# Performance work log

Measured on AMD Instinct MI355X. Metric: run time of the kernel, lower is better.

The kernel has to match this reference:

```python
import jax, jax.numpy as jnp
import numpy as np

NEG_INF = -1000000000.0
B, N, D, H, L, DFF = 4, 1024, 512, 8, 6, 2048
DH = D // H
R2 = 10.0 ** 2  # locality_radius^2
EPS = 1e-5


def setup_inputs() -> dict:
    key = jax.random.key(0)
    ks = jax.random.split(key, 16)
    s = 0.02
    inp = {
        "tokens": jax.random.normal(ks[0], (B, N, D), jnp.float32),
        "xy": jax.random.uniform(ks[1], (B, N, 2), jnp.float32) * 100.0,
        "Wq": jax.random.normal(ks[2], (L, D, D), jnp.float32) * s,
        "Wk": jax.random.normal(ks[3], (L, D, D), jnp.float32) * s,
        "Wv": jax.random.normal(ks[4], (L, D, D), jnp.float32) * s,
        "Wo": jax.random.normal(ks[5], (L, D, D), jnp.float32) * s,
        "bo": jnp.zeros((L, D), jnp.float32),
        "W1": jax.random.normal(ks[6], (L, D, DFF), jnp.float32) * s,
        "b1": jnp.zeros((L, DFF), jnp.float32),
        "W2": jax.random.normal(ks[7], (L, DFF, D), jnp.float32) * s,
        "b2": jnp.zeros((L, D), jnp.float32),
        "g1": jnp.ones((L, D), jnp.float32),
        "be1": jnp.zeros((L, D), jnp.float32),
        "g2": jnp.ones((L, D), jnp.float32),
        "be2": jnp.zeros((L, D), jnp.float32),
        "gf": jnp.ones((D,), jnp.float32),
        "bf": jnp.zeros((D,), jnp.float32),
        "alive": jax.random.randint(ks[8], (B, N), 0, 2, dtype=jnp.int32),
        "species": jax.random.randint(ks[9], (B, N), 0, 3, dtype=jnp.int32),
        "n_agents": 512,
    }
    return inp


def _ln(x, g, b):
    m = jnp.mean(x, axis=-1, keepdims=True)
    v = jnp.mean((x - m) ** 2, axis=-1, keepdims=True)
    return (x - m) * jax.lax.rsqrt(v + EPS) * g + b


def _build_bias(alive, xy, species, dtype):
    # (B,1,N,N) additive bias, broadcast over heads (original repeats per head)
    af = alive.astype(dtype)
    bias = (1.0 - af)[:, None, None, :] * NEG_INF  # dead keys
    d2 = jnp.sum((xy[:, :, None, :] - xy[:, None, :, :]) ** 2, axis=-1)  # (B,N,N)
    bias = bias + jnp.where(d2 > R2, NEG_INF, 0.0)[:, None, :, :]
    ia = species < 2
    ip = species == 2
    ct = (ia[:, :, None] & ip[:, None, :]) | (ip[:, :, None] & ia[:, None, :])
    bias = bias + jnp.where(ct, NEG_INF, 0.0)[:, None, :, :]
    return bias


def reference(tokens, xy, Wq, Wk, Wv, Wo, bo, W1, b1, W2, b2,
              g1, be1, g2, be2, gf, bf, alive, species, n_agents):
    bias = _build_bias(alive, xy, species, tokens.dtype)
    scale = np.float32(np.sqrt(DH))
    x = tokens
    for l in range(L):
        h = _ln(x, g1[l], be1[l])
        q = (h @ Wq[l]).reshape(B, N, H, DH)
        k = (h @ Wk[l]).reshape(B, N, H, DH)
        v = (h @ Wv[l]).reshape(B, N, H, DH)
        scores = jnp.einsum('bihd,bjhd->bhij', q, k) / scale + bias
        w = jax.nn.softmax(scores, axis=-1)
        o = jnp.einsum('bhij,bjhd->bihd', w, v).reshape(B, N, D)
        x = x + (o @ Wo[l] + bo[l])
        h2 = _ln(x, g2[l], be2[l])
        ff = jax.nn.gelu(h2 @ W1[l] + b1[l], approximate=False) @ W2[l] + b2[l]
        x = x + ff
    return _ln(x, gf, bf)
```

## Files before the change

kernel.cpp:

```cpp
#include <hip/hip_runtime.h>
#include <math.h>

namespace {

constexpr int B = 4, N = 1024, D = 512, H = 8, DHd = 64, L = 6, DFFd = 2048;
constexpr int M = B * N;
constexpr int QKVS = 3 * D;
constexpr float NEG = -1000000000.0f;
constexpr float R2c = 100.0f;

typedef __attribute__((ext_vector_type(8))) short bf16x8;
typedef __attribute__((ext_vector_type(4))) float f32x4;
typedef __attribute__((ext_vector_type(16))) float f32x16;

__device__ __forceinline__ short f2bf(float f) {
  union { float f; unsigned u; } c; c.f = f;
  unsigned r = (c.u + 0x7fffu + ((c.u >> 16) & 1u)) >> 16;
  return (short)r;
}

__device__ __forceinline__ float gelu_f(float x) {
  return 0.5f * x * (1.0f + erff(x * 0.70710678118654752f));
}

__global__ __launch_bounds__(256) void bias_kernel(
    const float* __restrict__ xy, const int* __restrict__ alive,
    const int* __restrict__ species, float* __restrict__ bias)
{
  int j = blockIdx.x * 256 + threadIdx.x;
  int i = blockIdx.y;
  int b = blockIdx.z;
  float xi = xy[((size_t)b * N + i) * 2 + 0];
  float yi = xy[((size_t)b * N + i) * 2 + 1];
  float xj = xy[((size_t)b * N + j) * 2 + 0];
  float yj = xy[((size_t)b * N + j) * 2 + 1];
  float dx = xi - xj, dy = yi - yj;
  float d2 = dx * dx + dy * dy;
  float bv = 0.0f;
  if (alive[b * N + j] == 0) bv += NEG;
  if (d2 > R2c) bv += NEG;
  int si = species[b * N + i], sj = species[b * N + j];
  bool ia = si < 2, ip = si == 2, ja = sj < 2, jp = sj == 2;
  if ((ia && jp) || (ip && ja)) bv += NEG;
  bias[((size_t)b * N + i) * N + j] = bv;
}

__global__ __launch_bounds__(256) void wprep_kernel(
    const float* __restrict__ src, short* __restrict__ dst,
    int K, int Nc, size_t srcLS, size_t dstLS)
{
  __shared__ float t[32][33];
  int k0 = blockIdx.x * 32, n0 = blockIdx.y * 32;
  src += (size_t)blockIdx.z * srcLS;
  dst += (size_t)blockIdx.z * dstLS;
  int r = threadIdx.x >> 5, c = threadIdx.x & 31;
#pragma unroll
  for (int i = 0; i < 4; ++i)
    t[r + i * 8][c] = src[(size_t)(k0 + r + i * 8) * Nc + n0 + c];
  __syncthreads();
#pragma unroll
  for (int i = 0; i < 4; ++i)
    dst[(size_t)(n0 + r + i * 8) * K + k0 + c] = f2bf(t[c][r + i * 8]);
}

__global__ __launch_bounds__(64) void ln_kernel(
    const float* __restrict__ x, const float* __restrict__ g,
    const float* __restrict__ be, float* __restrict__ outf,
    short* __restrict__ outb)
{
  int row = blockIdx.x;
  int tid = threadIdx.x;
  const float* xr = x + (size_t)row * D;
  float v[8];
  float sum = 0.f;
#pragma unroll
  for (int i = 0; i < 8; ++i) { v[i] = xr[tid + i * 64]; sum += v[i]; }
#pragma unroll
  for (int off = 32; off > 0; off >>= 1) sum += __shfl_down(sum, off);
  sum = __shfl(sum, 0);
  float mean = sum * (1.0f / D);
  float vs = 0.f;
#pragma unroll
  for (int i = 0; i < 8; ++i) { float d = v[i] - mean; vs += d * d; }
#pragma unroll
  for (int off = 32; off > 0; off >>= 1) vs += __shfl_down(vs, off);
  vs = __shfl(vs, 0);
  float rstd = rsqrtf(vs * (1.0f / D) + 1e-5f);
#pragma unroll
  for (int i = 0; i < 8; ++i) {
    int c = tid + i * 64;
    float o = (v[i] - mean) * rstd * g[c] + be[c];
    if (outb) outb[(size_t)row * D + c] = f2bf(o);
    else      outf[(size_t)row * D + c] = o;
  }
}

__global__ __launch_bounds__(256, 2) void gemm_sk_kernel(
    const short* __restrict__ A, const short* __restrict__ Bt,
    const float* __restrict__ bvec, float* __restrict__ Cf,
    short* __restrict__ Cb, int K, int Nc, int mode)
{
  __shared__ __align__(16) char smem[4 * 17408];
  const int bm = blockIdx.y * 64, bn = blockIdx.x * 64;
  const int t = threadIdx.x, wave = t >> 6, lane = t & 63;
  const int half = lane >> 5;
  const int l32 = lane & 31;
  const int srow4 = lane >> 2, sseg4 = lane & 3;

  char* slot = smem + wave * 17408;
  const int kw0 = wave * (K >> 2);
  const int nch = K >> 7;

  const short* Ab = A + (size_t)(bm + srow4) * K + kw0 + sseg4 * 8;
  const short* Bb = Bt + (size_t)(bn + srow4) * K + kw0 + sseg4 * 8;

  auto issue = [&](int p, int kc) {
    char* ab = slot + p * 8192;
    char* bb = slot + p * 8192 + 4096;
#pragma unroll
    for (int i = 0; i < 4; ++i) {
      __builtin_amdgcn_global_load_lds(
          (const __attribute__((address_space(1))) void*)(Ab + (size_t)i * 16 * K + kc),
          (__attribute__((address_space(3))) void*)(ab + i * 1024), 16, 0, 0);
    }
#pragma unroll
    for (int i = 0; i < 4; ++i) {
      __builtin_amdgcn_global_load_lds(
          (const __attribute__((address_space(1))) void*)(Bb + (size_t)i * 16 * K + kc),
          (__attribute__((address_space(3))) void*)(bb + i * 1024), 16, 0, 0);
    }
  };

  f32x16 acc[2][2];
#pragma unroll
  for (int i = 0; i < 2; ++i)
#pragma unroll
    for (int j = 0; j < 2; ++j)
#pragma unroll
      for (int r = 0; r < 16; ++r) acc[i][j][r] = 0.f;

  issue(0, 0);
  for (int c = 0; c < nch; ++c) {
    const int p = c & 1;
    if (c + 1 < nch) {
      issue(p ^ 1, (c + 1) * 32);
      asm volatile("s_waitcnt vmcnt(%0)" :: "i"(8) : "memory");
    } else {
      asm volatile("s_waitcnt vmcnt(0)" ::: "memory");
    }
    const short* As = (const short*)(slot + p * 8192);
    const short* Bs = (const short*)(slot + p * 8192 + 4096);
#pragma unroll
    for (int ks = 0; ks < 2; ++ks) {
      bf16x8 a0 = *(const bf16x8*)&As[(l32) * 32 + ks * 16 + half * 8];
      bf16x8 a1 = *(const bf16x8*)&As[(32 + l32) * 32 + ks * 16 + half * 8];
      bf16x8 b0 = *(const bf16x8*)&Bs[(l32) * 32 + ks * 16 + half * 8];
      bf16x8 b1 = *(const bf16x8*)&Bs[(32 + l32) * 32 + ks * 16 + half * 8];
      acc[0][0] = __builtin_amdgcn_mfma_f32_32x32x16_bf16(a0, b0, acc[0][0], 0, 0, 0);
      acc[0][1] = __builtin_amdgcn_mfma_f32_32x32x16_bf16(a0, b1, acc[0][1], 0, 0, 0);
      acc[1][0] = __builtin_amdgcn_mfma_f32_32x32x16_bf16(a1, b0, acc[1][0], 0, 0, 0);
      acc[1][1] = __builtin_amdgcn_mfma_f32_32x32x16_bf16(a1, b1, acc[1][1], 0, 0, 0);
    }
  }

  float* red = (float*)slot;
#pragma unroll
  for (int ti = 0; ti < 2; ++ti)
#pragma unroll
    for (int tj = 0; tj < 2; ++tj)
#pragma unroll
      for (int r = 0; r < 16; ++r) {
        int row = ti * 32 + (r & 3) + 8 * (r >> 2) + 4 * half;
        red[row * 68 + tj * 32 + l32] = acc[ti][tj][r];
      }
  __syncthreads();

  const int row = t >> 2, cs = (t & 3) * 16;
  const size_t orow = (size_t)(bm + row) * Nc + bn + cs;
#pragma unroll
  for (int u = 0; u < 4; ++u) {
    float4 s0 = *(const float4*)((const float*)(smem + 0 * 17408) + row * 68 + cs + u * 4);
    float4 s1 = *(const float4*)((const float*)(smem + 1 * 17408) + row * 68 + cs + u * 4);
    float4 s2 = *(const float4*)((const float*)(smem + 2 * 17408) + row * 68 + cs + u * 4);
    float4 s3 = *(const float4*)((const float*)(smem + 3 * 17408) + row * 68 + cs + u * 4);
    float o0 = s0.x + s1.x + s2.x + s3.x;
    float o1 = s0.y + s1.y + s2.y + s3.y;
    float o2 = s0.z + s1.z + s2.z + s3.z;
    float o3 = s0.w + s1.w + s2.w + s3.w;
    const int col = bn + cs + u * 4;
    if (mode == 0) {
      short4 w = {f2bf(o0), f2bf(o1), f2bf(o2), f2bf(o3)};
      *(short4*)&Cb[orow + u * 4] = w;
    } else if (mode == 1) {
      float4 bv = *(const float4*)&bvec[col];
      float4 rv = *(const float4*)&Cf[orow + u * 4];
      float4 w = {o0 + bv.x + rv.x, o1 + bv.y + rv.y, o2 + bv.z + rv.z, o3 + bv.w + rv.w};
      *(float4*)&Cf[orow + u * 4] = w;
    } else {
      float4 bv = *(const float4*)&bvec[col];
      short4 w = {f2bf(gelu_f(o0 + bv.x)), f2bf(gelu_f(o1 + bv.y)),
                  f2bf(gelu_f(o2 + bv.z)), f2bf(gelu_f(o3 + bv.w))};
      *(short4*)&Cb[orow + u * 4] = w;
    }
  }
}

__global__ __launch_bounds__(256) void attn_mfma_kernel(
    const short* __restrict__ qkv, const float* __restrict__ bias,
    short* __restrict__ o)
{
  constexpr int LDR = 72;
  __shared__ __align__(16) short Qs[64 * LDR];
  __shared__ __align__(16) short Ks[2][64 * LDR];
  __shared__ __align__(16) short Vt[2][64 * LDR];
  __shared__ __align__(16) short Ps[4 * 16 * LDR];

  const int q0 = blockIdx.x * 64;
  const int hh = blockIdx.y;
  const int b  = blockIdx.z;
  const int t  = threadIdx.x;
  const int wave = t >> 6;
  const int lane = t & 63;
  const int quad = lane >> 4;
  const int ln16 = lane & 15;
  const int srow = t >> 2, sseg = t & 3;

  {
    const short* qb = qkv + (size_t)(b * N + q0 + srow) * QKVS + hh * 64 + sseg * 16;
    *(bf16x8*)&Qs[srow * LDR + sseg * 16] = *(const bf16x8*)qb;
    *(bf16x8*)&Qs[srow * LDR + sseg * 16 + 8] = *(const bf16x8*)(qb + 8);
  }
  __syncthreads();

  const int qrow = wave * 16 + ln16;
  const bf16x8 qf0 = *(const bf16x8*)&Qs[qrow * LDR + quad * 8];
  const bf16x8 qf1 = *(const bf16x8*)&Qs[qrow * LDR + 32 + quad * 8];

  float m_run = -1e30f, l_run = 0.f;
  f32x4 Oacc[4];
#pragma unroll
  for (int dt = 0; dt < 4; ++dt) Oacc[dt] = (f32x4){0.f, 0.f, 0.f, 0.f};

  short* Psw = Ps + wave * 16 * LDR;
  const float* brow = bias + (size_t)(b * N + q0 + wave * 16 + ln16) * N;
  const short* kb0 = qkv + (size_t)b * N * QKVS + 512 + hh * 64 + sseg * 16;
  const short* vb0 = qkv + (size_t)b * N * QKVS + 1024 + hh * 64 + sseg * 16;

  bf16x8 k0r = *(const bf16x8*)(kb0 + (size_t)srow * QKVS);
  bf16x8 k1r = *(const bf16x8*)(kb0 + (size_t)srow * QKVS + 8);
  bf16x8 v0r = *(const bf16x8*)(vb0 + (size_t)srow * QKVS);
  bf16x8 v1r = *(const bf16x8*)(vb0 + (size_t)srow * QKVS + 8);
  float4 b4[4];
#pragma unroll
  for (int ks = 0; ks < 4; ++ks)
    b4[ks] = *(const float4*)&brow[ks * 16 + quad * 4];

  for (int kt = 0; kt < 16; ++kt) {
    const int p = kt & 1;
    *(bf16x8*)&Ks[p][srow * LDR + sseg * 16] = k0r;
    *(bf16x8*)&Ks[p][srow * LDR + sseg * 16 + 8] = k1r;
#pragma unroll
    for (int e = 0; e < 8; ++e) {
      Vt[p][(sseg * 16 + e) * LDR + srow] = v0r[e];
      Vt[p][(sseg * 16 + 8 + e) * LDR + srow] = v1r[e];
    }
    const int k0n = (kt + 1 < 16) ? (kt + 1) * 64 : 0;
    bf16x8 nk0 = *(const bf16x8*)(kb0 + (size_t)(k0n + srow) * QKVS);
    bf16x8 nk1 = *(const bf16x8*)(kb0 + (size_t)(k0n + srow) * QKVS + 8);
    bf16x8 nv0 = *(const bf16x8*)(vb0 + (size_t)(k0n + srow) * QKVS);
    bf16x8 nv1 = *(const bf16x8*)(vb0 + (size_t)(k0n + srow) * QKVS + 8);
    float4 bcur[4] = {b4[0], b4[1], b4[2], b4[3]};
#pragma unroll
    for (int ks = 0; ks < 4; ++ks)
      b4[ks] = *(const float4*)&brow[k0n + ks * 16 + quad * 4];
    asm volatile("s_waitcnt lgkmcnt(0)\n\ts_barrier" ::: "memory");

    float sv[4][4];
#pragma unroll
    for (int ks = 0; ks < 4; ++ks) {
      bf16x8 a0 = *(const bf16x8*)&Ks[p][(ks * 16 + ln16) * LDR + quad * 8];
      bf16x8 a1 = *(const bf16x8*)&Ks[p][(ks * 16 + ln16) * LDR + 32 + quad * 8];
      f32x4 z = (f32x4){0.f, 0.f, 0.f, 0.f};
      z = __builtin_amdgcn_mfma_f32_16x16x32_bf16(a0, qf0, z, 0, 0, 0);
      z = __builtin_amdgcn_mfma_f32_16x16x32_bf16(a1, qf1, z, 0, 0, 0);
#pragma unroll
      for (int r = 0; r < 4; ++r)
        sv[ks][r] = z[r] * 0.125f + (&bcur[ks].x)[r];
    }

    float mt = sv[0][0];
#pragma unroll
    for (int ks = 0; ks < 4; ++ks)
#pragma unroll
      for (int r = 0; r < 4; ++r) mt = fmaxf(mt, sv[ks][r]);
    mt = fmaxf(mt, __shfl_xor(mt, 16));
    mt = fmaxf(mt, __shfl_xor(mt, 32));
    const float m_new = fmaxf(m_run, mt);
    const float alpha = __expf(m_run - m_new);
    m_run = m_new;
    float rs = 0.f;
    float pv[4][4];
#pragma unroll
    for (int ks = 0; ks < 4; ++ks)
#pragma unroll
      for (int r = 0; r < 4; ++r) {
        float e = __expf(sv[ks][r] - m_new);
        pv[ks][r] = e;
        rs += e;
      }
    rs += __shfl_xor(rs, 16);
    rs += __shfl_xor(rs, 32);
    l_run = l_run * alpha + rs;
    float af[4];
#pragma unroll
    for (int r = 0; r < 4; ++r) af[r] = __shfl(alpha, quad * 4 + r);
#pragma unroll
    for (int dt = 0; dt < 4; ++dt)
#pragma unroll
      for (int r = 0; r < 4; ++r) Oacc[dt][r] *= af[r];

#pragma unroll
    for (int ks = 0; ks < 4; ++ks) {
      short4 pk = {f2bf(pv[ks][0]), f2bf(pv[ks][1]), f2bf(pv[ks][2]), f2bf(pv[ks][3])};
      *(short4*)&Psw[ln16 * LDR + ks * 16 + quad * 4] = pk;
    }

    bf16x8 ap0 = *(const bf16x8*)&Psw[ln16 * LDR + quad * 8];
    bf16x8 ap1 = *(const bf16x8*)&Psw[ln16 * LDR + 32 + quad * 8];
#pragma unroll
    for (int dt = 0; dt < 4; ++dt) {
      bf16x8 bv0 = *(const bf16x8*)&Vt[p][(dt * 16 + ln16) * LDR + quad * 8];
      bf16x8 bv1 = *(const bf16x8*)&Vt[p][(dt * 16 + ln16) * LDR + 32 + quad * 8];
      Oacc[dt] = __builtin_amdgcn_mfma_f32_16x16x32_bf16(ap0, bv0, Oacc[dt], 0, 0, 0);
      Oacc[dt] = __builtin_amdgcn_mfma_f32_16x16x32_bf16(ap1, bv1, Oacc[dt], 0, 0, 0);
    }

    k0r = nk0; k1r = nk1; v0r = nv0; v1r = nv1;
  }

  const float linv = 1.0f / l_run;
  float iv[4];
#pragma unroll
  for (int r = 0; r < 4; ++r) iv[r] = __shfl(linv, quad * 4 + r);
#pragma unroll
  for (int dt = 0; dt < 4; ++dt) {
#pragma unroll
    for (int r = 0; r < 4; ++r) {
      int row = q0 + wave * 16 + quad * 4 + r;
      o[(size_t)(b * N + row) * D + hh * 64 + dt * 16 + ln16] =
          f2bf(Oacc[dt][r] * iv[r]);
    }
  }
}

}

extern "C" void kernel_launch(void* const* d_in, const int* in_sizes, int n_in,
                              void* d_out, int out_size, void* d_ws, size_t ws_size,
                              hipStream_t stream)
{
  const float* tokens  = (const float*)d_in[0];
  const float* xy      = (const float*)d_in[1];
  const float* Wq      = (const float*)d_in[2];
  const float* Wk      = (const float*)d_in[3];
  const float* Wv      = (const float*)d_in[4];
  const float* Wo      = (const float*)d_in[5];
  const float* bo      = (const float*)d_in[6];
  const float* W1      = (const float*)d_in[7];
  const float* b1      = (const float*)d_in[8];
  const float* W2      = (const float*)d_in[9];
  const float* b2      = (const float*)d_in[10];
  const float* g1      = (const float*)d_in[11];
  const float* be1     = (const float*)d_in[12];
  const float* g2      = (const float*)d_in[13];
  const float* be2     = (const float*)d_in[14];
  const float* gf      = (const float*)d_in[15];
  const float* bf      = (const float*)d_in[16];
  const int*   alive   = (const int*)d_in[17];
  const int*   species = (const int*)d_in[18];

  char* p = (char*)d_ws;
  float* bias = (float*)p; p += (size_t)B * N * N * 4;
  float* x    = (float*)p; p += (size_t)M * D * 4;
  short* h    = (short*)p; p += (size_t)M * D * 2;
  short* qkv  = (short*)p; p += (size_t)M * DFFd * 2;
  short* ff   = qkv;
  short* Wqkvt = (short*)p; p += (size_t)L * QKVS * D * 2;
  short* Wot   = (short*)p; p += (size_t)L * D * D * 2;
  short* W1t   = (short*)p; p += (size_t)L * DFFd * D * 2;
  short* W2t   = (short*)p; p += (size_t)L * D * DFFd * 2;

  hipMemcpyAsync(x, tokens, sizeof(float) * (size_t)M * D,
                 hipMemcpyDeviceToDevice, stream);
  bias_kernel<<<dim3(N / 256, N, B), 256, 0, stream>>>(xy, alive, species, bias);

  wprep_kernel<<<dim3(16, 16, L), 256, 0, stream>>>(
      Wq, Wqkvt + (size_t)0 * D * D, D, D, (size_t)D * D, (size_t)QKVS * D);
  wprep_kernel<<<dim3(16, 16, L), 256, 0, stream>>>(
      Wk, Wqkvt + (size_t)1 * D * D, D, D, (size_t)D * D, (size_t)QKVS * D);
  wprep_kernel<<<dim3(16, 16, L), 256, 0, stream>>>(
      Wv, Wqkvt + (size_t)2 * D * D, D, D, (size_t)D * D, (size_t)QKVS * D);
  wprep_kernel<<<dim3(16, 16, L), 256, 0, stream>>>(
      Wo, Wot, D, D, (size_t)D * D, (size_t)D * D);
  wprep_kernel<<<dim3(16, 64, L), 256, 0, stream>>>(
      W1, W1t, D, DFFd, (size_t)D * DFFd, (size_t)DFFd * D);
  wprep_kernel<<<dim3(64, 16, L), 256, 0, stream>>>(
      W2, W2t, DFFd, D, (size_t)DFFd * D, (size_t)D * DFFd);

  for (int l = 0; l < L; ++l) {
    ln_kernel<<<M, 64, 0, stream>>>(x, g1 + l * D, be1 + l * D, nullptr, h);
    gemm_sk_kernel<<<dim3(QKVS / 64, M / 64), 256, 0, stream>>>(
        h, Wqkvt + (size_t)l * QKVS * D, nullptr, nullptr, qkv, D, QKVS, 0);
    attn_mfma_kernel<<<dim3(N / 64, H, B), 256, 0, stream>>>(qkv, bias, h);
    gemm_sk_kernel<<<dim3(D / 64, M / 64), 256, 0, stream>>>(
        h, Wot + (size_t)l * D * D, bo + l * D, x, nullptr, D, D, 1);
    ln_kernel<<<M, 64, 0, stream>>>(x, g2 + l * D, be2 + l * D, nullptr, h);
    gemm_sk_kernel<<<dim3(DFFd / 64, M / 64), 256, 0, stream>>>(
        h, W1t + (size_t)l * DFFd * D, b1 + l * DFFd, nullptr, ff, D, DFFd, 2);
    gemm_sk_kernel<<<dim3(D / 64, M / 64), 256, 0, stream>>>(
        ff, W2t + (size_t)l * D * DFFd, b2 + l * D, x, nullptr, DFFd, D, 1);
  }
  ln_kernel<<<M, 64, 0, stream>>>(x, gf, bf, (float*)d_out, nullptr);
}
```

Baseline: 992.3 us.

## Fuse prep kernels, swizzle GEMM LDS, remap workgroups for XCD locality

Merges the weight transpose/convert kernels, the bias build and the token copy into one prep launch. Adds an XOR swizzle to the GEMM's LDS tile layout to cut bank conflicts on fragment reads. Remaps GEMM and attention workgroup indices so neighbouring tiles land on the same XCD for better L2 reuse. Packs four LayerNorm rows per 256-thread block. Costs are extra index arithmetic and a large branchy prep kernel.

```diff
diff --git a/kernel.cpp b/kernel.cpp
--- a/kernel.cpp
+++ b/kernel.cpp
@@ -3,7 +3,7 @@
 
 namespace {
 
-constexpr int B = 4, N = 1024, D = 512, H = 8, DHd = 64, L = 6, DFFd = 2048;
+constexpr int B = 4, N = 1024, D = 512, H = 8, L = 6, DFFd = 2048;
 constexpr int M = B * N;
 constexpr int QKVS = 3 * D;
 constexpr float NEG = -1000000000.0f;
@@ -23,53 +23,79 @@
   return 0.5f * x * (1.0f + erff(x * 0.70710678118654752f));
 }
 
-__global__ __launch_bounds__(256) void bias_kernel(
+__global__ __launch_bounds__(256) void prep_kernel(
+    const float* __restrict__ Wq, const float* __restrict__ Wk,
+    const float* __restrict__ Wv, const float* __restrict__ Wo,
+    const float* __restrict__ W1, const float* __restrict__ W2,
+    short* __restrict__ Wqkvt, short* __restrict__ Wot,
+    short* __restrict__ W1t, short* __restrict__ W2t,
     const float* __restrict__ xy, const int* __restrict__ alive,
-    const int* __restrict__ species, float* __restrict__ bias)
+    const int* __restrict__ species, float* __restrict__ bias,
+    const float* __restrict__ tokens, float* __restrict__ x)
 {
-  int j = blockIdx.x * 256 + threadIdx.x;
-  int i = blockIdx.y;
-  int b = blockIdx.z;
-  float xi = xy[((size_t)b * N + i) * 2 + 0];
-  float yi = xy[((size_t)b * N + i) * 2 + 1];
-  float xj = xy[((size_t)b * N + j) * 2 + 0];
-  float yj = xy[((size_t)b * N + j) * 2 + 1];
-  float dx = xi - xj, dy = yi - yj;
-  float d2 = dx * dx + dy * dy;
-  float bv = 0.0f;
-  if (alive[b * N + j] == 0) bv += NEG;
-  if (d2 > R2c) bv += NEG;
-  int si = species[b * N + i], sj = species[b * N + j];
-  bool ia = si < 2, ip = si == 2, ja = sj < 2, jp = sj == 2;
-  if ((ia && jp) || (ip && ja)) bv += NEG;
-  bias[((size_t)b * N + i) * N + j] = bv;
-}
-
-__global__ __launch_bounds__(256) void wprep_kernel(
-    const float* __restrict__ src, short* __restrict__ dst,
-    int K, int Nc, size_t srcLS, size_t dstLS)
-{
-  __shared__ float t[32][33];
-  int k0 = blockIdx.x * 32, n0 = blockIdx.y * 32;
-  src += (size_t)blockIdx.z * srcLS;
-  dst += (size_t)blockIdx.z * dstLS;
-  int r = threadIdx.x >> 5, c = threadIdx.x & 31;
-#pragma unroll
-  for (int i = 0; i < 4; ++i)
-    t[r + i * 8][c] = src[(size_t)(k0 + r + i * 8) * Nc + n0 + c];
-  __syncthreads();
-#pragma unroll
-  for (int i = 0; i < 4; ++i)
-    dst[(size_t)(n0 + r + i * 8) * K + k0 + c] = f2bf(t[c][r + i * 8]);
-}
-
-__global__ __launch_bounds__(64) void ln_kernel(
+  __shared__ float tt[32][33];
+  const int blk = blockIdx.x;
+  const int t = threadIdx.x;
+
+  if (blk < 18432) {
+    const float* src; short* dst; int K, Nc, tx; size_t srcLS, dstLS; int lb;
+    if (blk < 6144) {
+      const int w = blk / 1536; lb = blk % 1536; tx = 16; K = 512; Nc = 512;
+      srcLS = (size_t)D * D;
+      if (w == 0)      { src = Wq; dst = Wqkvt; dstLS = (size_t)QKVS * D; }
+      else if (w == 1) { src = Wk; dst = Wqkvt + (size_t)D * D; dstLS = (size_t)QKVS * D; }
+      else if (w == 2) { src = Wv; dst = Wqkvt + (size_t)2 * D * D; dstLS = (size_t)QKVS * D; }
+      else             { src = Wo; dst = Wot; dstLS = (size_t)D * D; }
+    } else if (blk < 12288) {
+      lb = blk - 6144; tx = 16; K = 512; Nc = DFFd;
+      src = W1; dst = W1t; srcLS = (size_t)D * DFFd; dstLS = (size_t)DFFd * D;
+    } else {
+      lb = blk - 12288; tx = 64; K = DFFd; Nc = 512;
+      src = W2; dst = W2t; srcLS = (size_t)DFFd * D; dstLS = (size_t)D * DFFd;
+    }
+    const int per = (K / 32) * (Nc / 32);
+    const int z = lb / per, rem = lb % per;
+    const int k0 = (rem % tx) * 32, n0 = (rem / tx) * 32;
+    src += (size_t)z * srcLS; dst += (size_t)z * dstLS;
+    const int r = t >> 5, c = t & 31;
+#pragma unroll
+    for (int i = 0; i < 4; ++i)
+      tt[r + i * 8][c] = src[(size_t)(k0 + r + i * 8) * Nc + n0 + c];
+    __syncthreads();
+#pragma unroll
+    for (int i = 0; i < 4; ++i)
+      dst[(size_t)(n0 + r + i * 8) * K + k0 + c] = f2bf(tt[c][r + i * 8]);
+  } else if (blk < 34816) {
+    const int e = blk - 18432;
+    const int j = (e & 3) * 256 + t;
+    const int i = (e >> 2) & 1023;
+    const int b = e >> 12;
+    float xi = xy[((size_t)b * N + i) * 2 + 0];
+    float yi = xy[((size_t)b * N + i) * 2 + 1];
+    float xj = xy[((size_t)b * N + j) * 2 + 0];
+    float yj = xy[((size_t)b * N + j) * 2 + 1];
+    float dx = xi - xj, dy = yi - yj;
+    float d2 = dx * dx + dy * dy;
+    float bv = 0.0f;
+    if (alive[b * N + j] == 0) bv += NEG;
+    if (d2 > R2c) bv += NEG;
+    int si = species[b * N + i], sj = species[b * N + j];
+    bool ia = si < 2, ip = si == 2, ja = sj < 2, jp = sj == 2;
+    if ((ia && jp) || (ip && ja)) bv += NEG;
+    bias[((size_t)b * N + i) * N + j] = bv;
+  } else {
+    const size_t e = (size_t)(blk - 34816) * 256 + t;
+    ((float4*)x)[e] = ((const float4*)tokens)[e];
+  }
+}
+
+__global__ __launch_bounds__(256) void ln_kernel(
     const float* __restrict__ x, const float* __restrict__ g,
     const float* __restrict__ be, float* __restrict__ outf,
     short* __restrict__ outb)
 {
-  int row = blockIdx.x;
-  int tid = threadIdx.x;
+  int row = blockIdx.x * 4 + (threadIdx.x >> 6);
+  int tid = threadIdx.x & 63;
   const float* xr = x + (size_t)row * D;
   float v[8];
   float sum = 0.f;
@@ -101,11 +127,16 @@
     short* __restrict__ Cb, int K, int Nc, int mode)
 {
   __shared__ __align__(16) char smem[4 * 17408];
-  const int bm = blockIdx.y * 64, bn = blockIdx.x * 64;
+  const int gx = gridDim.x;
+  const int nwg = gx * gridDim.y;
+  const int f0 = blockIdx.y * gx + blockIdx.x;
+  const int f = (f0 & 7) * (nwg >> 3) + (f0 >> 3);
+  const int bm = (f / gx) * 64, bn = (f % gx) * 64;
   const int t = threadIdx.x, wave = t >> 6, lane = t & 63;
   const int half = lane >> 5;
   const int l32 = lane & 31;
-  const int srow4 = lane >> 2, sseg4 = lane & 3;
+  const int srow4 = lane >> 2;
+  const int sseg4 = (lane & 3) ^ ((lane >> 3) & 3);
 
   char* slot = smem + wave * 17408;
   const int kw0 = wave * (K >> 2);
@@ -118,18 +149,21 @@
     char* ab = slot + p * 8192;
     char* bb = slot + p * 8192 + 4096;
 #pragma unroll
-    for (int i = 0; i < 4; ++i) {
+    for (int i = 0; i < 4; ++i)
       __builtin_amdgcn_global_load_lds(
           (const __attribute__((address_space(1))) void*)(Ab + (size_t)i * 16 * K + kc),
           (__attribute__((address_space(3))) void*)(ab + i * 1024), 16, 0, 0);
-    }
-#pragma unroll
-    for (int i = 0; i < 4; ++i) {
+#pragma unroll
+    for (int i = 0; i < 4; ++i)
       __builtin_amdgcn_global_load_lds(
           (const __attribute__((address_space(1))) void*)(Bb + (size_t)i * 16 * K + kc),
           (__attribute__((address_space(3))) void*)(bb + i * 1024), 16, 0, 0);
-    }
   };
+
+  const int key = (l32 >> 1) & 3;
+  int offs[2];
+#pragma unroll
+  for (int ks = 0; ks < 2; ++ks) offs[ks] = ((ks * 2 + half) ^ key) * 8;
 
   f32x16 acc[2][2];
 #pragma unroll
@@ -144,7 +178,7 @@
     const int p = c & 1;
     if (c + 1 < nch) {
       issue(p ^ 1, (c + 1) * 32);
-      asm volatile("s_waitcnt vmcnt(%0)" :: "i"(8) : "memory");
+      asm volatile("s_waitcnt vmcnt(8)" ::: "memory");
     } else {
       asm volatile("s_waitcnt vmcnt(0)" ::: "memory");
     }
@@ -152,10 +186,10 @@
     const short* Bs = (const short*)(slot + p * 8192 + 4096);
 #pragma unroll
     for (int ks = 0; ks < 2; ++ks) {
-      bf16x8 a0 = *(const bf16x8*)&As[(l32) * 32 + ks * 16 + half * 8];
-      bf16x8 a1 = *(const bf16x8*)&As[(32 + l32) * 32 + ks * 16 + half * 8];
-      bf16x8 b0 = *(const bf16x8*)&Bs[(l32) * 32 + ks * 16 + half * 8];
-      bf16x8 b1 = *(const bf16x8*)&Bs[(32 + l32) * 32 + ks * 16 + half * 8];
+      bf16x8 a0 = *(const bf16x8*)&As[(l32) * 32 + offs[ks]];
+      bf16x8 a1 = *(const bf16x8*)&As[(32 + l32) * 32 + offs[ks]];
+      bf16x8 b0 = *(const bf16x8*)&Bs[(l32) * 32 + offs[ks]];
+      bf16x8 b1 = *(const bf16x8*)&Bs[(32 + l32) * 32 + offs[ks]];
       acc[0][0] = __builtin_amdgcn_mfma_f32_32x32x16_bf16(a0, b0, acc[0][0], 0, 0, 0);
       acc[0][1] = __builtin_amdgcn_mfma_f32_32x32x16_bf16(a0, b1, acc[0][1], 0, 0, 0);
       acc[1][0] = __builtin_amdgcn_mfma_f32_32x32x16_bf16(a1, b0, acc[1][0], 0, 0, 0);
@@ -215,9 +249,11 @@
   __shared__ __align__(16) short Vt[2][64 * LDR];
   __shared__ __align__(16) short Ps[4 * 16 * LDR];
 
-  const int q0 = blockIdx.x * 64;
-  const int hh = blockIdx.y;
-  const int b  = blockIdx.z;
+  const int f0 = blockIdx.x;
+  const int f  = (f0 & 7) * 64 + (f0 >> 3);
+  const int hh = f & 7;
+  const int q0 = ((f >> 3) & 15) * 64;
+  const int b  = f >> 7;
   const int t  = threadIdx.x;
   const int wave = t >> 6;
   const int lane = t & 63;
@@ -390,35 +426,22 @@
   short* W1t   = (short*)p; p += (size_t)L * DFFd * D * 2;
   short* W2t   = (short*)p; p += (size_t)L * D * DFFd * 2;
 
-  hipMemcpyAsync(x, tokens, sizeof(float) * (size_t)M * D,
-                 hipMemcpyDeviceToDevice, stream);
-  bias_kernel<<<dim3(N / 256, N, B), 256, 0, stream>>>(xy, alive, species, bias);
-
-  wprep_kernel<<<dim3(16, 16, L), 256, 0, stream>>>(
-      Wq, Wqkvt + (size_t)0 * D * D, D, D, (size_t)D * D, (size_t)QKVS * D);
-  wprep_kernel<<<dim3(16, 16, L), 256, 0, stream>>>(
-      Wk, Wqkvt + (size_t)1 * D * D, D, D, (size_t)D * D, (size_t)QKVS * D);
-  wprep_kernel<<<dim3(16, 16, L), 256, 0, stream>>>(
-      Wv, Wqkvt + (size_t)2 * D * D, D, D, (size_t)D * D, (size_t)QKVS * D);
-  wprep_kernel<<<dim3(16, 16, L), 256, 0, stream>>>(
-      Wo, Wot, D, D, (size_t)D * D, (size_t)D * D);
-  wprep_kernel<<<dim3(16, 64, L), 256, 0, stream>>>(
-      W1, W1t, D, DFFd, (size_t)D * DFFd, (size_t)DFFd * D);
-  wprep_kernel<<<dim3(64, 16, L), 256, 0, stream>>>(
-      W2, W2t, DFFd, D, (size_t)DFFd * D, (size_t)D * DFFd);
+  prep_kernel<<<36864, 256, 0, stream>>>(
+      Wq, Wk, Wv, Wo, W1, W2, Wqkvt, Wot, W1t, W2t,
+      xy, alive, species, bias, tokens, x);
 
   for (int l = 0; l < L; ++l) {
-    ln_kernel<<<M, 64, 0, stream>>>(x, g1 + l * D, be1 + l * D, nullptr, h);
+    ln_kernel<<<M / 4, 256, 0, stream>>>(x, g1 + l * D, be1 + l * D, nullptr, h);
     gemm_sk_kernel<<<dim3(QKVS / 64, M / 64), 256, 0, stream>>>(
         h, Wqkvt + (size_t)l * QKVS * D, nullptr, nullptr, qkv, D, QKVS, 0);
-    attn_mfma_kernel<<<dim3(N / 64, H, B), 256, 0, stream>>>(qkv, bias, h);
+    attn_mfma_kernel<<<dim3(N / 64 * H * B), 256, 0, stream>>>(qkv, bias, h);
     gemm_sk_kernel<<<dim3(D / 64, M / 64), 256, 0, stream>>>(
         h, Wot + (size_t)l * D * D, bo + l * D, x, nullptr, D, D, 1);
-    ln_kernel<<<M, 64, 0, stream>>>(x, g2 + l * D, be2 + l * D, nullptr, h);
+    ln_kernel<<<M / 4, 256, 0, stream>>>(x, g2 + l * D, be2 + l * D, nullptr, h);
     gemm_sk_kernel<<<dim3(DFFd / 64, M / 64), 256, 0, stream>>>(
         h, W1t + (size_t)l * DFFd * D, b1 + l * DFFd, nullptr, ff, D, DFFd, 2);
     gemm_sk_kernel<<<dim3(D / 64, M / 64), 256, 0, stream>>>(
         ff, W2t + (size_t)l * D * DFFd, b2 + l * D, x, nullptr, DFFd, D, 1);
   }
-  ln_kernel<<<M, 64, 0, stream>>>(x, gf, bf, (float*)d_out, nullptr);
-}
+  ln_kernel<<<M / 4, 256, 0, stream>>>(x, gf, bf, (float*)d_out, nullptr);
+}
```

Result: faster. 909.2 us (median of 2 runs) (-8.4%).
